# Kernel tuning notes

Hardware: AMD Instinct MI355X
Metric: run time of the kernel (lower is better)

Reference implementation:

```python
import jax, jax.numpy as jnp
import numpy as np

D = (96, 96, 96)          # per-item tensor shape (input_shape)
BATCH = 8
R1, R2 = 32, 16           # ranks for the two multi-resolution partitions
MAX_ITER = 15             # fixed ALS iteration count (torch default 100 w/ early stop)


def setup_inputs() -> dict:
    key = jax.random.key(0)
    k = jax.random.split(key, 5)
    m, n = D[0], D[1] * D[2]  # unfold: (first mode, rest) -> (96, 9216)
    return {
        "x": jax.random.normal(k[0], (BATCH,) + D, dtype=jnp.float32),
        "A0_1": jax.random.normal(k[1], (m, R1), dtype=jnp.float32),
        "B0_1": jax.random.normal(k[2], (n, R1), dtype=jnp.float32),
        "A0_2": jax.random.normal(k[3], (m, R2), dtype=jnp.float32),
        "B0_2": jax.random.normal(k[4], (n, R2), dtype=jnp.float32),
    }


def _clean(f):
    # torch.nan_to_num(f, nan=0.0, posinf=1e10, neginf=-1e10)
    return jnp.nan_to_num(f, nan=0.0, posinf=1e10, neginf=-1e10)


def _als(X, A, B):
    """2-mode PARAFAC == ALS matrix factorization. X: (m,n), A: (m,r), B: (n,r)."""
    def step(carry, _):
        A, B = carry
        # mode 0: khatri-rao prod is just B; V = B^T B; A = (X B) pinv(V)
        A = _clean((X @ B) @ jnp.linalg.pinv(B.T @ B))
        # mode 1: unfold is X^T; V = A^T A; B = (X^T A) pinv(V)
        B = _clean((X.T @ A) @ jnp.linalg.pinv(A.T @ A))
        return (A, B), None
    (A, B), _ = jax.lax.scan(step, (A, B), None, length=MAX_ITER)
    return A, B


def _per_item(t, A0_1, B0_1, A0_2, B0_2):
    m = D[0]
    # partition 1 ([[0],[1,2]]): unfold -> (96, 9216)
    X1 = t.reshape(m, -1)
    A1, B1 = _als(X1, A0_1, B0_1)
    approx1 = (A1 @ B1.T).reshape(D)
    residual = t - approx1
    # partition 2 ([[0,1],[2]]): same identity mode order -> same unfold shape
    X2 = residual.reshape(m, -1)
    A2, B2 = _als(X2, A0_2, B0_2)
    approx2 = (A2 @ B2.T).reshape(D)
    # reconstruct() = sum of partition approximations
    return approx1 + approx2


def reference(x, A0_1, B0_1, A0_2, B0_2):
    # per-item MRLR reconstruction, vmapped over the batch (torch loops per item)
    return jax.vmap(_per_item, in_axes=(0, None, None, None, None))(
        x, A0_1, B0_1, A0_2, B0_2
    )
```

## Files before the change

### kernel.cpp

```cpp
#include <hip/hip_runtime.h>


#define TID ((int)threadIdx.x)
typedef float4 f4;

#define SC27 (1.0f/134217728.0f)

__device__ __forceinline__ f4 ld4(const float* p) { return *(const f4*)p; }
__device__ __forceinline__ void st4(float* p, f4 v) { *(f4*)p = v; }
__device__ __forceinline__ f4 f4zero() { return make_float4(0.f,0.f,0.f,0.f); }
__device__ __forceinline__ f4 add4(f4 a, f4 b){ return make_float4(a.x+b.x,a.y+b.y,a.z+b.z,a.w+b.w); }
__device__ __forceinline__ f4 sub4(f4 a, f4 b){ return make_float4(a.x-b.x,a.y-b.y,a.z-b.z,a.w-b.w); }
__device__ __forceinline__ f4 scl4(f4 a, float s){ return make_float4(a.x*s,a.y*s,a.z*s,a.w*s); }
__device__ __forceinline__ void fma4(f4& a, float s, f4 v) {
  a.x = fmaf(s,v.x,a.x); a.y = fmaf(s,v.y,a.y); a.z = fmaf(s,v.z,a.z); a.w = fmaf(s,v.w,a.w);
}
__device__ __forceinline__ float dot4(f4 a, f4 b, float acc) {
  acc = fmaf(a.x,b.x,acc); acc = fmaf(a.y,b.y,acc);
  acc = fmaf(a.z,b.z,acc); acc = fmaf(a.w,b.w,acc); return acc;
}
__device__ __forceinline__ void trimap(int t, int& ti, int& tj) {
  int rem = t; ti = 0;
  #pragma unroll
  for (int r = 0; r < 12; ++r) { int w = 12 - r; if (rem < w) { ti = r; break; } rem -= w; }
  tj = ti + rem;
}
__device__ __forceinline__ void init8(f4 acc[8][2]) {
  #pragma unroll
  for (int a = 0; a < 8; ++a) { acc[a][0] = f4zero(); acc[a][1] = f4zero(); }
}
__device__ __forceinline__ void tile8_step(f4 acc[8][2], const float* u, const float* v) {
  f4 u0 = ld4(u), u1 = ld4(u+4), v0 = ld4(v), v1 = ld4(v+4);
  float aa[8] = {u0.x,u0.y,u0.z,u0.w,u1.x,u1.y,u1.z,u1.w};
  #pragma unroll
  for (int a = 0; a < 8; ++a) { fma4(acc[a][0], aa[a], v0); fma4(acc[a][1], aa[a], v1); }
}

__global__ __launch_bounds__(512) void k1_partials(
    const float* __restrict__ x, const float* __restrict__ b01,
    const float* __restrict__ b02, float* __restrict__ part,
    int nch, int nsc) {
  __shared__ __align__(16) float Xst[48][100];
  __shared__ __align__(16) float Bs[48][52];
  __shared__ __align__(16) float red[9600];
  int bid = blockIdx.x;
  int item = bid & 7, kc = bid >> 3;
  const float* X = x + (size_t)item * 96 * 9216;
  float* base = part + (size_t)(item * nch + kc) * 9600;

  int t = TID, kh = 0, tt = 0;
  const float* ap = nullptr; const float* bp = nullptr;
  float* op = nullptr; int os = 0; bool isM = false;
  bool active = (t < 450);
  if (active) {
    kh = t / 150; tt = t % 150;
    if (tt < 78) {
      int ti, tj; trimap(tt, ti, tj);
      ap = &Xst[0][ti*8]; bp = &Xst[0][tj*8];
      op = base + tt*64; os = 8; isM = true;
    } else {
      int u = tt - 78; int i0 = (u/6)*8, c0 = (u%6)*8;
      ap = &Xst[0][i0]; bp = &Bs[0][c0];
      op = base + 4992 + i0*48 + c0; os = 48;
    }
  }

  f4 acc[8][2]; init8(acc);

  for (int sc = 0; sc < nsc; ++sc) {
    int k0 = (kc * nsc + sc) * 48;
    __syncthreads();
    for (int e = TID; e < 1152; e += 512) {
      int i = e / 12, kq = (e % 12) * 4;
      f4 v = ld4(&X[(size_t)i * 9216 + k0 + kq]);
      Xst[kq][i] = v.x; Xst[kq+1][i] = v.y; Xst[kq+2][i] = v.z; Xst[kq+3][i] = v.w;
    }
    for (int e = TID; e < 384; e += 512) {
      int kk = e / 8, cq = (e % 8) * 4;
      st4(&Bs[kk][cq], ld4(&b01[(size_t)(k0 + kk) * 32 + cq]));
    }
    for (int e = TID; e < 192; e += 512) {
      int kk = e / 4, cq = (e % 4) * 4;
      st4(&Bs[kk][32+cq], ld4(&b02[(size_t)(k0 + kk) * 16 + cq]));
    }
    __syncthreads();
    if (active) {
      int asr = 100, bsr = isM ? 100 : 52;
      const float* ar = ap + kh * asr;
      const float* br = bp + kh * bsr;
      #pragma unroll 4
      for (int kk = kh; kk < 48; kk += 3) {
        tile8_step(acc, ar, br);
        ar += 3 * asr; br += 3 * bsr;
      }
    }
  }
  __syncthreads();
  if (active && kh == 1) {
    #pragma unroll
    for (int a = 0; a < 8; ++a) { st4(&red[tt*64+a*8], acc[a][0]); st4(&red[tt*64+a*8+4], acc[a][1]); }
  }
  __syncthreads();
  if (active && kh == 0) {
    #pragma unroll
    for (int a = 0; a < 8; ++a) {
      acc[a][0] = add4(acc[a][0], ld4(&red[tt*64+a*8]));
      acc[a][1] = add4(acc[a][1], ld4(&red[tt*64+a*8+4]));
    }
  }
  __syncthreads();
  if (active && kh == 2) {
    #pragma unroll
    for (int a = 0; a < 8; ++a) { st4(&red[tt*64+a*8], acc[a][0]); st4(&red[tt*64+a*8+4], acc[a][1]); }
  }
  __syncthreads();
  if (active && kh == 0) {
    #pragma unroll
    for (int a = 0; a < 8; ++a) {
      f4 s0 = add4(acc[a][0], ld4(&red[tt*64+a*8]));
      f4 s1 = add4(acc[a][1], ld4(&red[tt*64+a*8+4]));
      st4(op + a*os, s0); st4(op + a*os + 4, s1);
    }
  }
}

__global__ __launch_bounds__(128) void k2_reduce(
    const float* __restrict__ part, float* __restrict__ Mb,
    float* __restrict__ Cb, int nch) {
  int bid = blockIdx.x;
  int item = bid & 7, chunk = bid >> 3;
  if (TID >= 120) return;
  int q4 = chunk * 120 + TID;
  int off = q4 * 4;
  const float* p = part + (size_t)item * nch * 9600 + off;
  f4 s = f4zero();
  #pragma unroll 8
  for (int c = 0; c < nch; ++c) s = add4(s, ld4(p + (size_t)c * 9600));
  if (off < 4992) {
    int tile = off >> 6, w = (off & 63) >> 2;
    int r = w >> 1, cq = (w & 1) * 4;
    int ti, tj; trimap(tile, ti, tj);
    int i = ti*8 + r, j = tj*8 + cq;
    float* Mi = Mb + (size_t)item * 9216;
    st4(&Mi[i*96 + j], s);
    Mi[(j+0)*96 + i] = s.x; Mi[(j+1)*96 + i] = s.y;
    Mi[(j+2)*96 + i] = s.z; Mi[(j+3)*96 + i] = s.w;
  } else {
    st4(&Cb[(size_t)item * 4608 + (off - 4992)], s);
  }
}

__global__ __launch_bounds__(256) void kw_phase(
    const float* __restrict__ Ag, const float* __restrict__ Bg,
    const float* __restrict__ Subg, float* __restrict__ Dg, float scale,
    const float* __restrict__ Tin, int ti_istr, int tis, int tsub,
    float* __restrict__ Tout, int to_istr, int tos, int TW) {
  __shared__ __align__(16) float Bs[96][100];
  __shared__ __align__(16) float As[8][100];
  __shared__ __align__(16) float Ts[96][36];
  int bid = blockIdx.x;
  int item = bid & 7, w = bid >> 3, t = TID;
  const float* A = Ag + (size_t)item * 9216;

  if (w < 12) {
    const float* B = Bg + (size_t)item * 9216;
    for (int e = t; e < 2304; e += 256) {
      int r = e / 24, cq = (e % 24) * 4;
      st4(&Bs[r][cq], ld4(&B[r*96 + cq]));
    }
    if (t < 192) {
      int r = t / 24, cq = (t % 24) * 4;
      st4(&As[r][cq], ld4(&A[(size_t)(w*8 + r)*96 + cq]));
    }
    __syncthreads();
    if (t < 192) {
      int rl = t / 24, jb = (t % 24) * 4;
      f4 acc = f4zero();
      #pragma unroll 8
      for (int k = 0; k < 96; ++k) fma4(acc, As[rl][k], ld4(&Bs[k][jb]));
      int r = w*8 + rl;
      if (Subg) acc = sub4(ld4(&Subg[(size_t)item*9216 + r*96 + jb]), acc);
      else      acc = scl4(acc, scale);
      st4(&Dg[(size_t)item*9216 + r*96 + jb], acc);
    }
  } else {
    for (int e = t; e < 2304; e += 256) {
      int r = e / 24, cq = (e % 24) * 4;
      st4(&Bs[r][cq], ld4(&A[r*96 + cq]));
    }
    int nq = TW >> 2;
    const float* Ti = Tin + (size_t)item * ti_istr;
    for (int e = t; e < 96*nq; e += 256) {
      int r = e / nq, cq = (e % nq) * 4;
      st4(&Ts[r][cq], ld4(&Ti[(size_t)r * tis + cq]));
    }
    __syncthreads();
    int nact = (TW == 32) ? 192 : 96;
    if (t < nact) {
      int r  = (TW == 32) ? (t >> 1) : t;
      int c0 = (TW == 32) ? (t & 1) * 16 : 0;
      f4 acc[4] = {f4zero(), f4zero(), f4zero(), f4zero()};
      #pragma unroll 4
      for (int k = 0; k < 96; ++k) {
        float a = Bs[r][k];
        const float* tr = &Ts[k][c0];
        fma4(acc[0], a, ld4(tr));   fma4(acc[1], a, ld4(tr+4));
        fma4(acc[2], a, ld4(tr+8)); fma4(acc[3], a, ld4(tr+12));
      }
      if (tsub) {
        #pragma unroll
        for (int u = 0; u < 4; ++u) acc[u] = sub4(ld4(&Ts[r][c0 + u*4]), acc[u]);
      }
      float* To = Tout + (size_t)item * to_istr;
      #pragma unroll
      for (int u = 0; u < 4; ++u) st4(&To[(size_t)r * tos + c0 + u*4], acc[u]);
    }
  }
}

template<int R>
__device__ void gj_wave(float* aug, int lane) {
  float col[R];
  if (lane < R) {
    #pragma unroll
    for (int i = 0; i < R; ++i) col[i] = aug[i*68 + lane];
  } else {
    #pragma unroll
    for (int i = 0; i < R; ++i) col[i] = (i == lane - R) ? 1.f : 0.f;
  }
  #pragma unroll
  for (int c = 0; c < R; ++c) {
    float pc = __shfl(col[c], c);
    float rp = 1.f / pc;
    bool isc = (lane == c);
    #pragma unroll
    for (int i = 0; i < R; ++i) {
      if (i == c) continue;
      float fi = __shfl(col[i], c) * rp;
      float v = fmaf(-fi, col[c], col[i]);
      col[i] = isc ? 0.f : v;
    }
  }
  #pragma unroll
  for (int i = 0; i < R; ++i) {
    float d = __shfl(col[i], i);
    col[i] = col[i] / d;
  }
  if (lane >= R) {
    #pragma unroll
    for (int i = 0; i < R; ++i) aug[i*68 + lane] = col[i];
  }
}

template<int TW>
__global__ __launch_bounds__(256) void kB_chain(
    const float* __restrict__ Sg, const float* __restrict__ Yg,
    float* __restrict__ Qg, float* __restrict__ QKg) {
  __shared__ __align__(16) float smem[18688];
  float* St  = smem;
  float* Ta  = smem + 9600;
  float* Tb  = smem + 13056;
  float* aug = smem + 16512;

  int item = blockIdx.x, t = TID;
  const float* S = Sg + (size_t)item * 9216;
  const float* Y = Yg + (size_t)item * 3072;
  float* Qo  = Qg  + (size_t)item * 3072;
  float* QKo = QKg + (size_t)item * 3072;
  const int nq = TW >> 2;

  for (int e = t; e < 2304; e += 256) {
    int r = e / 24, cq = (e % 24) * 4;
    f4 v = ld4(&S[r*96 + cq]);
    St[(cq+0)*100 + r] = v.x; St[(cq+1)*100 + r] = v.y;
    St[(cq+2)*100 + r] = v.z; St[(cq+3)*100 + r] = v.w;
  }
  for (int e = t; e < 96*nq; e += 256) {
    int r = e / nq, cq = (e % nq) * 4;
    st4(&Ta[r*36 + cq], ld4(&Y[r*32 + cq]));
  }
  __syncthreads();

  #pragma unroll
  for (int pass = 0; pass < 3; ++pass) {
    const float* src = (pass & 1) ? Tb : Ta;
    float* dst       = (pass & 1) ? Ta : Tb;
    int ntask = 24 * nq;
    if (t < ntask) {
      int rb = (t / nq) * 4, c4 = (t % nq) * 4;
      f4 acc[4] = {f4zero(), f4zero(), f4zero(), f4zero()};
      #pragma unroll 4
      for (int k = 0; k < 96; ++k) {
        f4 s = ld4(&St[k*100 + rb]);
        f4 v = ld4(&src[k*36 + c4]);
        fma4(acc[0], s.x, v); fma4(acc[1], s.y, v);
        fma4(acc[2], s.z, v); fma4(acc[3], s.w, v);
      }
      #pragma unroll
      for (int j = 0; j < 4; ++j) st4(&dst[(rb + j)*36 + c4], acc[j]);
    }
    __syncthreads();
  }

  {
    int na = TW >> 2;
    if (t < na*na) {
      int ab = (t / na) * 4, b4 = (t % na) * 4;
      f4 acc[4] = {f4zero(), f4zero(), f4zero(), f4zero()};
      #pragma unroll 4
      for (int k = 0; k < 96; ++k) {
        f4 qa = ld4(&Tb[k*36 + ab]);
        f4 qb = ld4(&Tb[k*36 + b4]);
        fma4(acc[0], qa.x, qb); fma4(acc[1], qa.y, qb);
        fma4(acc[2], qa.z, qb); fma4(acc[3], qa.w, qb);
      }
      #pragma unroll
      for (int j = 0; j < 4; ++j) st4(&aug[(ab + j)*68 + b4], acc[j]);
    }
  }
  __syncthreads();

  if (t < 2*TW) gj_wave<TW>(aug, t);
  __syncthreads();
  for (int e = t; e < TW*TW; e += 256) {
    int m = e / TW, c = e % TW;
    aug[c*68 + m] = aug[m*68 + TW + c];
  }
  __syncthreads();

  for (int e = t; e < 96*nq; e += 256) {
    int r = e / nq, c4 = (e % nq) * 4;
    f4 acc = f4zero();
    #pragma unroll
    for (int m4 = 0; m4 < TW; m4 += 4) {
      f4 qv = ld4(&Tb[r*36 + m4]);
      acc.x = dot4(qv, ld4(&aug[(c4+0)*68 + m4]), acc.x);
      acc.y = dot4(qv, ld4(&aug[(c4+1)*68 + m4]), acc.y);
      acc.z = dot4(qv, ld4(&aug[(c4+2)*68 + m4]), acc.z);
      acc.w = dot4(qv, ld4(&aug[(c4+3)*68 + m4]), acc.w);
    }
    st4(&QKo[r*32 + c4], acc);
    st4(&Qo[r*32 + c4], ld4(&Tb[r*36 + c4]));
  }
}

template<int TW, int MODE>
__global__ __launch_bounds__(256) void kC_wbuild(
    const float* __restrict__ Qg, const float* __restrict__ QKg,
    float* __restrict__ W1g, float* __restrict__ Tgg) {
  __shared__ __align__(16) float Qs[96][36];
  __shared__ __align__(16) float QKs[96][36];
  int bid = blockIdx.x;
  int item = bid & 7, w = bid >> 3, t = TID;
  const float* Q  = Qg  + (size_t)item * 3072;
  const float* QK = QKg + (size_t)item * 3072;
  float* W1 = W1g + (size_t)item * 9216;
  float* Tg = Tgg + (size_t)item * 9216;
  const int nq = TW >> 2;

  for (int e = t; e < 96*nq; e += 256) {
    int r = e / nq, cq = (e % nq) * 4;
    st4(&Qs[r][cq],  ld4(&Q[r*32 + cq]));
    st4(&QKs[r][cq], ld4(&QK[r*32 + cq]));
  }
  __syncthreads();

  if (t < 192) {
    int rr = t / 24, jb = (t % 24) * 4;
    int r = w*8 + rr;
    f4 acc = f4zero();
    #pragma unroll
    for (int c4 = 0; c4 < TW; c4 += 4) {
      f4 qk = ld4(&QKs[r][c4]);
      acc.x = dot4(qk, ld4(&Qs[jb+0][c4]), acc.x);
      acc.y = dot4(qk, ld4(&Qs[jb+1][c4]), acc.y);
      acc.z = dot4(qk, ld4(&Qs[jb+2][c4]), acc.z);
      acc.w = dot4(qk, ld4(&Qs[jb+3][c4]), acc.w);
    }
    if (MODE == 1) st4(&W1[r*96 + jb], acc);
    else           st4(&Tg[r*96 + jb], add4(acc, ld4(&W1[r*96 + jb])));
  }
}

__global__ __launch_bounds__(256) void k4_out(
    const float* __restrict__ x, const float* __restrict__ Tgg,
    float* __restrict__ out) {
  __shared__ __align__(16) float Tt[96][100];
  int bid = blockIdx.x;
  int item = bid & 7, jb = bid >> 3;
  const float* Tg = Tgg + (size_t)item * 9216;
  for (int e = TID * 4; e < 9216; e += 1024) {
    f4 v = ld4(&Tg[e]);
    int i = e / 96, k = e % 96;
    Tt[k][i] = v.x; Tt[k+1][i] = v.y; Tt[k+2][i] = v.z; Tt[k+3][i] = v.w;
  }
  __syncthreads();

  int jq = (TID % 32) * 4, ig = TID / 32;
  int i0 = ig * 12;
  int col = jb * 128 + jq;
  const float* X = x + (size_t)item * 96 * 9216;
  f4 acc[12];
  #pragma unroll
  for (int a = 0; a < 12; ++a) acc[a] = f4zero();

  for (int k = 0; k < 96; ++k) {
    f4 xv = ld4(&X[(size_t)k * 9216 + col]);
    f4 t0 = ld4(&Tt[k][i0]), t1 = ld4(&Tt[k][i0+4]), t2 = ld4(&Tt[k][i0+8]);
    fma4(acc[0], t0.x, xv); fma4(acc[1], t0.y, xv); fma4(acc[2], t0.z, xv); fma4(acc[3], t0.w, xv);
    fma4(acc[4], t1.x, xv); fma4(acc[5], t1.y, xv); fma4(acc[6], t1.z, xv); fma4(acc[7], t1.w, xv);
    fma4(acc[8], t2.x, xv); fma4(acc[9], t2.y, xv); fma4(acc[10], t2.z, xv); fma4(acc[11], t2.w, xv);
  }
  float* O = out + (size_t)item * 96 * 9216;
  #pragma unroll
  for (int a = 0; a < 12; ++a) st4(&O[(size_t)(i0 + a) * 9216 + col], acc[a]);
}

extern "C" void kernel_launch(void* const* d_in, const int* in_sizes, int n_in,
                              void* d_out, int out_size, void* d_ws, size_t ws_size,
                              hipStream_t stream) {
  (void)in_sizes; (void)n_in; (void)out_size;
  const float* x   = (const float*)d_in[0];
  const float* b01 = (const float*)d_in[2];
  const float* b02 = (const float*)d_in[4];
  float* out = (float*)d_out;
  float* ws  = (float*)d_ws;

  const size_t EXTRA = 73728ull*5 + 36864 + 24576*3 + 12288;
  int nch = (ws_size >= ((size_t)64*8*9600 + EXTRA) * sizeof(float)) ? 64 : 32;
  int nsc = 9216 / nch / 48;

  float* Mb  = ws + (size_t)nch * 8 * 9600;
  float* Cb  = Mb  + 73728;
  float* Sb  = Cb  + 36864;
  float* S2b = Sb  + 73728;
  float* W1b = S2b + 73728;
  float* Tgb = W1b + 73728;
  float* Yb  = Tgb + 73728;
  float* Qb  = Yb  + 24576;
  float* QKb = Qb  + 24576;
  float* CPb = QKb + 24576;

  k1_partials<<<dim3(nch*8), 512, 0, stream>>>(x, b01, b02, ws, nch, nsc);
  k2_reduce<<<dim3(160), 128, 0, stream>>>(ws, Mb, Cb, nch);

  kw_phase<<<dim3(96),256,0,stream>>>(Mb, Mb, nullptr, Sb, SC27,
      nullptr,0,0,0, nullptr,0,0, 0);
  kw_phase<<<dim3(104),256,0,stream>>>(Sb, Sb, nullptr, S2b, 1.f,
      Cb,4608,48,0, Yb,3072,32, 32);
  kB_chain<32><<<dim3(8),256,0,stream>>>(S2b, Yb, Qb, QKb);
  kC_wbuild<32,1><<<dim3(96),256,0,stream>>>(Qb, QKb, W1b, Tgb);

  kw_phase<<<dim3(104),256,0,stream>>>(W1b, Mb, Mb, Sb, 1.f,
      Cb+32,4608,48,1, CPb,1536,16, 16);
  kw_phase<<<dim3(96),256,0,stream>>>(Sb, W1b, Sb, Mb, 1.f,
      nullptr,0,0,0, nullptr,0,0, 0);

  kw_phase<<<dim3(96),256,0,stream>>>(Mb, Mb, nullptr, Sb, SC27,
      nullptr,0,0,0, nullptr,0,0, 0);
  kw_phase<<<dim3(104),256,0,stream>>>(Sb, Sb, nullptr, S2b, 1.f,
      CPb,1536,16,0, Yb,3072,32, 16);
  kB_chain<16><<<dim3(8),256,0,stream>>>(S2b, Yb, Qb, QKb);
  kC_wbuild<16,2><<<dim3(96),256,0,stream>>>(Qb, QKb, W1b, Tgb);

  k4_out<<<dim3(576), 256, 0, stream>>>(x, Tgb, out);
}
```

Measured before the change: 183.1 us.

## Split serial 8-block chain into wider squaring kernels plus small apply/gram kernels

Replaces the single-block-per-item kB_chain, which applied S three times serially and then built the Gram matrix, with an extra kw_phase squaring step run on 104 blocks (S^4 and its product with Y), a small kq_apply that multiplies by S^4, and a kf_gram kernel that splits the Gram reduction over two thread halves. The aim is to move most of the matrix-power work from an 8-block kernel onto a wider grid so latency-bound serial passes shrink. It adds two kernel launches per partition and needs more workspace, and computing S^4 explicitly may change rounding compared with repeated application.

Result: slower. 188.9 us (+3.2%).

```diff
diff --git a/kernel.cpp b/kernel.cpp
--- a/kernel.cpp
+++ b/kernel.cpp
@@ -218,12 +218,51 @@
   }
 }
 
+template<int TW>
+__global__ __launch_bounds__(256) void kq_apply(
+    const float* __restrict__ Ag, const float* __restrict__ Ting,
+    float* __restrict__ Qg) {
+  __shared__ __align__(16) float As[96][100];
+  __shared__ __align__(16) float Ts[96][36];
+  int item = blockIdx.x, t = TID;
+  const float* A  = Ag   + (size_t)item * 9216;
+  const float* Ti = Ting + (size_t)item * 3072;
+  float* Qo = Qg + (size_t)item * 3072;
+  const int nq = TW >> 2;
+
+  for (int e = t; e < 2304; e += 256) {
+    int r = e / 24, cq = (e % 24) * 4;
+    st4(&As[r][cq], ld4(&A[r*96 + cq]));
+  }
+  for (int e = t; e < 96*nq; e += 256) {
+    int r = e / nq, cq = (e % nq) * 4;
+    st4(&Ts[r][cq], ld4(&Ti[r*32 + cq]));
+  }
+  __syncthreads();
+
+  int nact = (TW == 32) ? 192 : 96;
+  if (t < nact) {
+    int r  = (TW == 32) ? (t >> 1) : t;
+    int c0 = (TW == 32) ? (t & 1) * 16 : 0;
+    f4 acc[4] = {f4zero(), f4zero(), f4zero(), f4zero()};
+    #pragma unroll 4
+    for (int k = 0; k < 96; ++k) {
+      float a = As[r][k];
+      const float* tr = &Ts[k][c0];
+      fma4(acc[0], a, ld4(tr));   fma4(acc[1], a, ld4(tr+4));
+      fma4(acc[2], a, ld4(tr+8)); fma4(acc[3], a, ld4(tr+12));
+    }
+    #pragma unroll
+    for (int u = 0; u < 4; ++u) st4(&Qo[r*32 + c0 + u*4], acc[u]);
+  }
+}
+
 template<int R>
-__device__ void gj_wave(float* aug, int lane) {
+__device__ void gj_wave(float (*aug)[68], int lane) {
   float col[R];
   if (lane < R) {
     #pragma unroll
-    for (int i = 0; i < R; ++i) col[i] = aug[i*68 + lane];
+    for (int i = 0; i < R; ++i) col[i] = aug[i][lane];
   } else {
     #pragma unroll
     for (int i = 0; i < R; ++i) col[i] = (i == lane - R) ? 1.f : 0.f;
@@ -248,74 +287,58 @@
   }
   if (lane >= R) {
     #pragma unroll
-    for (int i = 0; i < R; ++i) aug[i*68 + lane] = col[i];
+    for (int i = 0; i < R; ++i) aug[i][lane] = col[i];
   }
 }
 
 template<int TW>
-__global__ __launch_bounds__(256) void kB_chain(
-    const float* __restrict__ Sg, const float* __restrict__ Yg,
-    float* __restrict__ Qg, float* __restrict__ QKg) {
-  __shared__ __align__(16) float smem[18688];
-  float* St  = smem;
-  float* Ta  = smem + 9600;
-  float* Tb  = smem + 13056;
-  float* aug = smem + 16512;
-
+__global__ __launch_bounds__(256) void kf_gram(
+    const float* __restrict__ Qg, float* __restrict__ QKg) {
+  __shared__ __align__(16) float Qs[96][36];
+  __shared__ __align__(16) float aug[32][68];
+  __shared__ __align__(16) float red[32][36];
   int item = blockIdx.x, t = TID;
-  const float* S = Sg + (size_t)item * 9216;
-  const float* Y = Yg + (size_t)item * 3072;
-  float* Qo  = Qg  + (size_t)item * 3072;
+  const float* Q = Qg + (size_t)item * 3072;
   float* QKo = QKg + (size_t)item * 3072;
   const int nq = TW >> 2;
-
-  for (int e = t; e < 2304; e += 256) {
-    int r = e / 24, cq = (e % 24) * 4;
-    f4 v = ld4(&S[r*96 + cq]);
-    St[(cq+0)*100 + r] = v.x; St[(cq+1)*100 + r] = v.y;
-    St[(cq+2)*100 + r] = v.z; St[(cq+3)*100 + r] = v.w;
-  }
+  const int na = TW >> 2;
+
   for (int e = t; e < 96*nq; e += 256) {
     int r = e / nq, cq = (e % nq) * 4;
-    st4(&Ta[r*36 + cq], ld4(&Y[r*32 + cq]));
-  }
-  __syncthreads();
-
-  #pragma unroll
-  for (int pass = 0; pass < 3; ++pass) {
-    const float* src = (pass & 1) ? Tb : Ta;
-    float* dst       = (pass & 1) ? Ta : Tb;
-    int ntask = 24 * nq;
-    if (t < ntask) {
-      int rb = (t / nq) * 4, c4 = (t % nq) * 4;
+    st4(&Qs[r][cq], ld4(&Q[r*32 + cq]));
+  }
+  __syncthreads();
+
+  {
+    int nt = na*na;
+    if (t < 2*nt) {
+      int ch = t / nt, tt = t % nt;
+      int ab = (tt / na) * 4, b4 = (tt % na) * 4;
       f4 acc[4] = {f4zero(), f4zero(), f4zero(), f4zero()};
       #pragma unroll 4
-      for (int k = 0; k < 96; ++k) {
-        f4 s = ld4(&St[k*100 + rb]);
-        f4 v = ld4(&src[k*36 + c4]);
-        fma4(acc[0], s.x, v); fma4(acc[1], s.y, v);
-        fma4(acc[2], s.z, v); fma4(acc[3], s.w, v);
-      }
-      #pragma unroll
-      for (int j = 0; j < 4; ++j) st4(&dst[(rb + j)*36 + c4], acc[j]);
-    }
-    __syncthreads();
-  }
-
-  {
-    int na = TW >> 2;
-    if (t < na*na) {
-      int ab = (t / na) * 4, b4 = (t % na) * 4;
-      f4 acc[4] = {f4zero(), f4zero(), f4zero(), f4zero()};
-      #pragma unroll 4
-      for (int k = 0; k < 96; ++k) {
-        f4 qa = ld4(&Tb[k*36 + ab]);
-        f4 qb = ld4(&Tb[k*36 + b4]);
+      for (int k = ch*48; k < ch*48+48; ++k) {
+        f4 qa = ld4(&Qs[k][ab]);
+        f4 qb = ld4(&Qs[k][b4]);
         fma4(acc[0], qa.x, qb); fma4(acc[1], qa.y, qb);
         fma4(acc[2], qa.z, qb); fma4(acc[3], qa.w, qb);
       }
+      if (ch == 1) {
+        #pragma unroll
+        for (int j = 0; j < 4; ++j) st4(&red[ab + j][b4], acc[j]);
+      } else {
+        #pragma unroll
+        for (int j = 0; j < 4; ++j) st4(&aug[ab + j][b4], acc[j]);
+      }
+    }
+  }
+  __syncthreads();
+  {
+    int nt = na*na;
+    if (t < nt) {
+      int ab = (t / na) * 4, b4 = (t % na) * 4;
       #pragma unroll
-      for (int j = 0; j < 4; ++j) st4(&aug[(ab + j)*68 + b4], acc[j]);
+      for (int j = 0; j < 4; ++j)
+        st4(&aug[ab + j][b4], add4(ld4(&aug[ab + j][b4]), ld4(&red[ab + j][b4])));
     }
   }
   __syncthreads();
@@ -324,7 +347,7 @@
   __syncthreads();
   for (int e = t; e < TW*TW; e += 256) {
     int m = e / TW, c = e % TW;
-    aug[c*68 + m] = aug[m*68 + TW + c];
+    aug[c][m] = aug[m][TW + c];
   }
   __syncthreads();
 
@@ -333,14 +356,13 @@
     f4 acc = f4zero();
     #pragma unroll
     for (int m4 = 0; m4 < TW; m4 += 4) {
-      f4 qv = ld4(&Tb[r*36 + m4]);
-      acc.x = dot4(qv, ld4(&aug[(c4+0)*68 + m4]), acc.x);
-      acc.y = dot4(qv, ld4(&aug[(c4+1)*68 + m4]), acc.y);
-      acc.z = dot4(qv, ld4(&aug[(c4+2)*68 + m4]), acc.z);
-      acc.w = dot4(qv, ld4(&aug[(c4+3)*68 + m4]), acc.w);
+      f4 qv = ld4(&Qs[r][m4]);
+      acc.x = dot4(qv, ld4(&aug[c4+0][m4]), acc.x);
+      acc.y = dot4(qv, ld4(&aug[c4+1][m4]), acc.y);
+      acc.z = dot4(qv, ld4(&aug[c4+2][m4]), acc.z);
+      acc.w = dot4(qv, ld4(&aug[c4+3][m4]), acc.w);
     }
     st4(&QKo[r*32 + c4], acc);
-    st4(&Qo[r*32 + c4], ld4(&Tb[r*36 + c4]));
   }
 }
 
@@ -426,7 +448,7 @@
   float* out = (float*)d_out;
   float* ws  = (float*)d_ws;
 
-  const size_t EXTRA = 73728ull*5 + 36864 + 24576*3 + 12288;
+  const size_t EXTRA = 73728ull*6 + 36864 + 24576*4 + 12288;
   int nch = (ws_size >= ((size_t)64*8*9600 + EXTRA) * sizeof(float)) ? 64 : 32;
   int nsc = 9216 / nch / 48;
 
@@ -434,10 +456,12 @@
   float* Cb  = Mb  + 73728;
   float* Sb  = Cb  + 36864;
   float* S2b = Sb  + 73728;
-  float* W1b = S2b + 73728;
+  float* S4b = S2b + 73728;
+  float* W1b = S4b + 73728;
   float* Tgb = W1b + 73728;
-  float* Yb  = Tgb + 73728;
-  float* Qb  = Yb  + 24576;
+  float* Y1b = Tgb + 73728;
+  float* Y2b = Y1b + 24576;
+  float* Qb  = Y2b + 24576;
   float* QKb = Qb  + 24576;
   float* CPb = QKb + 24576;
 
@@ -447,8 +471,11 @@
   kw_phase<<<dim3(96),256,0,stream>>>(Mb, Mb, nullptr, Sb, SC27,
       nullptr,0,0,0, nullptr,0,0, 0);
   kw_phase<<<dim3(104),256,0,stream>>>(Sb, Sb, nullptr, S2b, 1.f,
-      Cb,4608,48,0, Yb,3072,32, 32);
-  kB_chain<32><<<dim3(8),256,0,stream>>>(S2b, Yb, Qb, QKb);
+      Cb,4608,48,0, Y1b,3072,32, 32);
+  kw_phase<<<dim3(104),256,0,stream>>>(S2b, S2b, nullptr, S4b, 1.f,
+      Y1b,3072,32,0, Y2b,3072,32, 32);
+  kq_apply<32><<<dim3(8),256,0,stream>>>(S4b, Y2b, Qb);
+  kf_gram<32><<<dim3(8),256,0,stream>>>(Qb, QKb);
   kC_wbuild<32,1><<<dim3(96),256,0,stream>>>(Qb, QKb, W1b, Tgb);
 
   kw_phase<<<dim3(104),256,0,stream>>>(W1b, Mb, Mb, Sb, 1.f,
@@ -459,8 +486,11 @@
   kw_phase<<<dim3(96),256,0,stream>>>(Mb, Mb, nullptr, Sb, SC27,
       nullptr,0,0,0, nullptr,0,0, 0);
   kw_phase<<<dim3(104),256,0,stream>>>(Sb, Sb, nullptr, S2b, 1.f,
-      CPb,1536,16,0, Yb,3072,32, 16);
-  kB_chain<16><<<dim3(8),256,0,stream>>>(S2b, Yb, Qb, QKb);
+      CPb,1536,16,0, Y1b,3072,32, 16);
+  kw_phase<<<dim3(104),256,0,stream>>>(S2b, S2b, nullptr, S4b, 1.f,
+      Y1b,3072,32,0, Y2b,3072,32, 16);
+  kq_apply<16><<<dim3(8),256,0,stream>>>(S4b, Y2b, Qb);
+  kf_gram<16><<<dim3(8),256,0,stream>>>(Qb, QKb);
   kC_wbuild<16,2><<<dim3(96),256,0,stream>>>(Qb, QKb, W1b, Tgb);
 
   k4_out<<<dim3(576), 256, 0, stream>>>(x, Tgb, out);
```
